# Kernel tuning notes

Hardware: AMD Instinct MI355X
Metric: run time of the kernel (lower is better)

## Reference

```python
import jax, jax.numpy as jnp
import numpy as np

B, N = 4096, 12
HID = 64
SLOPE = 0.2   # GATv2Conv default negative_slope
ALPHA = 0.1   # skip-connection scale


def _gabriel_adjacency(p):
    # p: [B, N, 2] node positions. Gabriel graph: edge (i,j) iff no other
    # point k lies inside the closed disk with diameter segment (p_i, p_j).
    n = p.shape[1]
    mid = (p[:, :, None, :] + p[:, None, :, :]) * 0.5                      # [B,N,N,2]
    r2 = jnp.sum((p[:, :, None, :] - p[:, None, :, :]) ** 2, -1) * 0.25    # [B,N,N]
    d2 = jnp.sum((p[:, None, None, :, :] - mid[:, :, :, None, :]) ** 2, -1)  # [B,i,j,k]
    eye = jnp.eye(n, dtype=bool)
    excl = eye[:, None, :] | eye[None, :, :]                               # k==i or k==j
    d2 = jnp.where(excl[None], jnp.inf, d2)
    gab = jnp.all(d2 > r2[..., None], axis=-1) & (~eye)[None]
    # undirected edges + self loops (GATv2Conv add_self_loops=True default)
    return gab | jnp.swapaxes(gab, 1, 2) | eye[None]                       # [B,N,N]


def _gatv2(x, adj, wl, wr, att, b):
    # PyG GATv2Conv, heads=1: e_ij = att . leaky_relu(W_l x_j + W_r x_i),
    # alpha = softmax_j(e_ij) over neighbors, out_i = sum_j alpha_ij W_l x_j + b.
    xl = x @ wl                                                            # source feats [B,N,H]
    xr = x @ wr                                                            # target feats [B,N,H]
    s = jax.nn.leaky_relu(xl[:, None, :, :] + xr[:, :, None, :], SLOPE)    # [B,i,j,H]
    e = jnp.einsum('bijh,h->bij', s, att)
    e = jnp.where(adj, e, -1e9)
    a = jax.nn.softmax(e, axis=-1)                                         # over sources j
    return jnp.einsum('bij,bjh->bih', a, xl) + b


def _forward(batch, enc_w1, enc_b1, enc_w2, enc_b2, enc_w3, enc_b3,
             g1_wl, g1_wr, g1_att, g1_b, g2_wl, g2_wr, g2_att, g2_b,
             g3_wl, g3_wr, g3_att, g3_b, g4_wl, g4_wr, g4_att, g4_b,
             lab_w, lab_b, val_w, val_b, skip_w, skip_b):
    h = jax.nn.relu(batch @ enc_w1 + enc_b1)
    h = jax.nn.relu(h @ enc_w2 + enc_b2)
    latent = h @ enc_w3 + enc_b3                                           # [B,N,3]
    # graph construction is non-differentiable (scipy in the original)
    adj = _gabriel_adjacency(jax.lax.stop_gradient(latent[..., :2]))
    x0 = latent[..., 2:3]                                                  # [B,N,1]
    x1 = jax.nn.relu(_gatv2(x0, adj, g1_wl, g1_wr, g1_att, g1_b))
    x2 = jax.nn.relu(_gatv2(x1, adj, g2_wl, g2_wr, g2_att, g2_b))
    skip = latent @ skip_w + skip_b
    x3 = jax.nn.relu(_gatv2(x2, adj, g3_wl, g3_wr, g3_att, g3_b) + ALPHA * skip)
    logits = x3 @ lab_w + lab_b                                            # [B,N,4]
    # note: original feeds x2 (not x3) into gcn4 -- kept faithful
    x4 = jax.nn.relu(_gatv2(x2, adj, g4_wl, g4_wr, g4_att, g4_b) + ALPHA * skip)
    values = x4 @ val_w + val_b                                            # [B,N,1]
    return batch[:, :, :4], batch[:, :, 4:5], logits, values, latent


def setup_inputs():
    key = jax.random.key(0)
    ks = iter(jax.random.split(key, 40))
    def rnd(shape, s=0.1):
        return jax.random.normal(next(ks), shape, dtype=jnp.float32) * s
    inp = {"batch": jax.random.normal(next(ks), (B, N, 5), dtype=jnp.float32)}
    inp.update(enc_w1=rnd((5, HID)), enc_b1=jnp.zeros((HID,), jnp.float32),
               enc_w2=rnd((HID, HID)), enc_b2=jnp.zeros((HID,), jnp.float32),
               enc_w3=rnd((HID, 3)), enc_b3=jnp.zeros((3,), jnp.float32))
    for i, cin in zip((1, 2, 3, 4), (1, HID, HID, HID)):
        inp[f"g{i}_wl"] = rnd((cin, HID)); inp[f"g{i}_wr"] = rnd((cin, HID))
        inp[f"g{i}_att"] = rnd((HID,)); inp[f"g{i}_b"] = jnp.zeros((HID,), jnp.float32)
    inp.update(lab_w=rnd((HID, 4)), lab_b=jnp.zeros((4,), jnp.float32),
               val_w=rnd((HID, 1)), val_b=jnp.zeros((1,), jnp.float32),
               skip_w=rnd((3, HID)), skip_b=jnp.zeros((HID,), jnp.float32))
    return inp


def reference(batch, enc_w1, enc_b1, enc_w2, enc_b2, enc_w3, enc_b3,
              g1_wl, g1_wr, g1_att, g1_b, g2_wl, g2_wr, g2_att, g2_b,
              g3_wl, g3_wr, g3_att, g3_b, g4_wl, g4_wr, g4_att, g4_b,
              lab_w, lab_b, val_w, val_b, skip_w, skip_b):
    return _forward(batch, enc_w1, enc_b1, enc_w2, enc_b2, enc_w3, enc_b3,
                    g1_wl, g1_wr, g1_att, g1_b, g2_wl, g2_wr, g2_att, g2_b,
                    g3_wl, g3_wr, g3_att, g3_b, g4_wl, g4_wr, g4_att, g4_b,
                    lab_w, lab_b, val_w, val_b, skip_w, skip_b)
```

## Files before the change

kernel.cpp:

```cpp
#include <hip/hip_runtime.h>
#include <hip/hip_bf16.h>
#include <math.h>

#define N     12
#define HID   64
#define STP   68
#define SLOPE 0.2f
#define ALPHA 0.1f

typedef float v2f __attribute__((ext_vector_type(2)));
typedef float v4f __attribute__((ext_vector_type(4)));
typedef int   i4  __attribute__((ext_vector_type(4)));
typedef short v8s __attribute__((ext_vector_type(8)));

static __device__ __forceinline__ v8s as_v8s(i4 v) {
    union { i4 a; v8s b; } u; u.a = v; return u.b;
}

#define OUT0 0
#define OUT1 196608
#define OUT2 245760
#define OUT3 442368
#define OUT4 491520

__global__ void prep_kernel(const float* __restrict__ enc_w2,
                            const float* __restrict__ g2_wl, const float* __restrict__ g2_wr,
                            const float* __restrict__ g3_wl, const float* __restrict__ g3_wr,
                            const float* __restrict__ g4_wl, const float* __restrict__ g4_wr,
                            const float* __restrict__ lab_w,
                            float* __restrict__ ws) {
    int t = threadIdx.x;
    int bx = blockIdx.x;
    if (bx < 64) {
        int c = bx;
        ws[t*64 + c] = enc_w2[c*64 + t];
        return;
    }
    if (bx == 112) {
        #pragma unroll
        for (int c = 0; c < 4; c++) ws[16384 + c*64 + t] = lab_w[t*4 + c];
        return;
    }
    int idx = bx - 64;
    int mat = idx >> 3, rem = idx & 7;
    int kt = rem >> 2, nt = rem & 3;
    const float* src;
    switch (mat) {
        case 0: src = g2_wl; break;
        case 1: src = g2_wr; break;
        case 2: src = g3_wl; break;
        case 3: src = g3_wr; break;
        case 4: src = g4_wl; break;
        default: src = g4_wr; break;
    }
    int quad = t >> 4, col = t & 15;
    int n = nt*16 + col;
    unsigned* dst = (unsigned*)(ws + 4096) + mat*2048 + (kt*4+nt)*256 + t*4;
    #pragma unroll
    for (int jp = 0; jp < 4; jp++) {
        int k0 = kt*32 + quad*8 + 2*jp;
        __hip_bfloat16 h0 = __float2bfloat16(src[(k0+0)*64 + n]);
        __hip_bfloat16 h1 = __float2bfloat16(src[(k0+1)*64 + n]);
        unsigned u0 = *(unsigned short*)&h0, u1 = *(unsigned short*)&h1;
        dst[jp] = u0 | (u1 << 16);
    }
}

template<bool TW>
__global__ __launch_bounds__(64, 3) void gae_kernel(
    const float* __restrict__ batch,
    const float* __restrict__ enc_w1, const float* __restrict__ enc_b1,
    const float* __restrict__ enc_w2, const float* __restrict__ enc_b2,
    const float* __restrict__ enc_w3, const float* __restrict__ enc_b3,
    const float* __restrict__ g1_wl, const float* __restrict__ g1_wr,
    const float* __restrict__ g1_att, const float* __restrict__ g1_b,
    const float* __restrict__ g2_wl, const float* __restrict__ g2_wr,
    const float* __restrict__ g2_att, const float* __restrict__ g2_b,
    const float* __restrict__ g3_wl, const float* __restrict__ g3_wr,
    const float* __restrict__ g3_att, const float* __restrict__ g3_b,
    const float* __restrict__ g4_wl, const float* __restrict__ g4_wr,
    const float* __restrict__ g4_att, const float* __restrict__ g4_b,
    const float* __restrict__ lab_w, const float* __restrict__ lab_b,
    const float* __restrict__ val_w, const float* __restrict__ val_b,
    const float* __restrict__ skip_w, const float* __restrict__ skip_b,
    const float* __restrict__ wsT,
    float* __restrict__ out)
{
    const int b = blockIdx.x;
    const int t = threadIdx.x;

    __shared__ __align__(16) float lds[2560];
    float* bufL = lds;
    float* bufR = lds + N*STP;
    float* xB   = lds + 2*N*STP;
    float* pool = lds + 2*N*STP + N*HID;
    unsigned char* pairs8 = (unsigned char*)&lds[2544];

    const v2f z2 = {0.f, 0.f};
    const v4f z4 = {0.f, 0.f, 0.f, 0.f};
    const v4f s4 = {SLOPE, SLOPE, SLOPE, SLOPE};

    const int p0 = t,        i0 = p0 / N, j0 = p0 - i0*N;
    const int p1 = t + 64,   i1 = p1 / N, j1 = p1 - i1*N;
    const int p2 = (t < 16) ? (t + 128) : 143;
    const int i2 = p2 / N,   j2 = p2 - i2*N;

    if (t < N*5) {
        float v = batch[b*(N*5) + t];
        pool[t] = v;
        int i = t / 5, f = t - i*5;
        if (f < 4) out[OUT0 + (size_t)b*(N*4) + i*4 + f] = v;
        else       out[OUT1 + (size_t)b*N + i] = v;
    }

    {
        float acc[N];
        float bias = enc_b1[t];
        #pragma unroll
        for (int i=0;i<N;i++) acc[i] = bias;
        #pragma unroll
        for (int f=0; f<5; f++) {
            float w = enc_w1[f*HID + t];
            #pragma unroll
            for (int i=0;i<N;i++) acc[i] = fmaf(pool[i*5+f], w, acc[i]);
        }
        #pragma unroll
        for (int i=0;i<N;i++) bufL[i*STP + t] = fmaxf(acc[i], 0.f);
    }

    {
        v2f acc[N];
        #pragma unroll
        for (int i=0;i<N;i++) acc[i] = z2;
        const float* w2p = TW ? (wsT + t*HID) : nullptr;
        for (int c=0;c<HID;c+=4) {
            v2f w01, w23;
            if (TW) {
                v4f w4 = *reinterpret_cast<const v4f*>(&w2p[c]);
                w01 = w4.xy; w23 = w4.zw;
            } else {
                w01 = (v2f){enc_w2[(c+0)*HID+t], enc_w2[(c+1)*HID+t]};
                w23 = (v2f){enc_w2[(c+2)*HID+t], enc_w2[(c+3)*HID+t]};
            }
            #pragma unroll
            for (int i=0;i<N;i++) {
                v4f xv = *reinterpret_cast<const v4f*>(&bufL[i*STP + c]);
                acc[i] = __builtin_elementwise_fma(xv.xy, w01, acc[i]);
                acc[i] = __builtin_elementwise_fma(xv.zw, w23, acc[i]);
            }
        }
        float bias = enc_b2[t];
        #pragma unroll
        for (int i=0;i<N;i++) bufR[i*STP + t] = fmaxf(bias + acc[i].x + acc[i].y, 0.f);
    }

    if (t < N*3) {
        int i = t / 3, c = t - i*3;
        float acc = enc_b3[c];
        for (int k=0;k<HID;k+=4) {
            v4f xv = *reinterpret_cast<const v4f*>(&bufR[i*STP + k]);
            acc = fmaf(xv.x, enc_w3[(k+0)*3+c], acc);
            acc = fmaf(xv.y, enc_w3[(k+1)*3+c], acc);
            acc = fmaf(xv.z, enc_w3[(k+2)*3+c], acc);
            acc = fmaf(xv.w, enc_w3[(k+3)*3+c], acc);
        }
        pool[t] = acc;
        out[OUT4 + (size_t)b*(N*3) + t] = acc;
    }

    float skipv[N];
    {
        float w0 = skip_w[t], w1 = skip_w[HID+t], w2 = skip_w[2*HID+t];
        float bias = skip_b[t];
        #pragma unroll
        for (int i=0;i<N;i++) {
            float v = bias;
            v = fmaf(pool[i*3+0], w0, v);
            v = fmaf(pool[i*3+1], w1, v);
            v = fmaf(pool[i*3+2], w2, v);
            skipv[i] = v;
        }
    }

    auto gab = [&](int i, int j)->bool {
        if (i == j) return false;
        float pix = pool[i*3], piy = pool[i*3+1];
        float pjx = pool[j*3], pjy = pool[j*3+1];
        float mx = (pix + pjx) * 0.5f, my = (piy + pjy) * 0.5f;
        float dx = pix - pjx, dy = piy - pjy;
        float r2 = (dx*dx + dy*dy) * 0.25f;
        bool g = true;
        #pragma unroll
        for (int k=0;k<N;k++) {
            float ex = pool[k*3] - mx, ey = pool[k*3+1] - my;
            bool ok = (k == i) || (k == j) || (ex*ex + ey*ey > r2);
            g = g && ok;
        }
        return g;
    };
    unsigned long long gb0 = __ballot(gab(i0, j0));
    unsigned long long gb1 = __ballot(gab(i1, j1));
    unsigned long long gb2 = __ballot((t < 16) && gab(i2, j2));
    auto gbit = [&](int p)->int {
        unsigned long long m = (p < 64) ? gb0 : ((p < 128) ? gb1 : gb2);
        return (int)((m >> (p & 63)) & 1ull);
    };
    const int adjA = gbit(p0) | gbit(j0*N+i0) | (i0 == j0);
    const int adjB = gbit(p1) | gbit(j1*N+i1) | (i1 == j1);
    const int adjC = (t < 16) ? (gbit(p2) | gbit(j2*N+i2) | (i2 == j2)) : 0;

    auto mbcnt64 = [&](unsigned long long m)->int {
        return __builtin_amdgcn_mbcnt_hi((unsigned)(m >> 32),
               __builtin_amdgcn_mbcnt_lo((unsigned)m, 0));
    };
    const unsigned long long am0 = __ballot(adjA != 0);
    const unsigned long long am1 = __ballot(adjB != 0);
    const unsigned long long am2 = __ballot(adjC != 0);
    const int c0  = __popcll(am0);
    const int c01 = c0 + __popcll(am1);
    const int nv  = c01 + __popcll(am2);
    const int idx0 = mbcnt64(am0);
    const int idx1 = c0  + mbcnt64(am1);
    const int idx2 = c01 + mbcnt64(am2);
    if (adjA)               pairs8[idx0] = (unsigned char)p0;
    if (adjB && idx1 < 64)  pairs8[idx1] = (unsigned char)p1;
    if (adjC && idx2 < 64)  pairs8[idx2] = (unsigned char)p2;
    const bool ovB = adjB && (idx1 >= 64);
    const bool ovC = adjC && (idx2 >= 64);
    const int nvc = nv < 64 ? nv : 64;

    auto scoreAt = [&](int i, int j, const float* __restrict__ att)->float {
        const float* Lj = &bufL[j*STP];
        const float* Ri = &bufR[i*STP];
        v4f a0 = z4, a1 = z4;
        for (int h=0; h<HID; h+=8) {
            v4f t0 = *reinterpret_cast<const v4f*>(&att[h]);
            v4f t1 = *reinterpret_cast<const v4f*>(&att[h+4]);
            v4f xl0 = *reinterpret_cast<const v4f*>(Lj + h);
            v4f xl1 = *reinterpret_cast<const v4f*>(Lj + h + 4);
            v4f xr0 = *reinterpret_cast<const v4f*>(Ri + h);
            v4f xr1 = *reinterpret_cast<const v4f*>(Ri + h + 4);
            v4f s0 = xl0 + xr0;
            v4f s1 = xl1 + xr1;
            v4f l0 = __builtin_elementwise_fma(s4, __builtin_elementwise_min(s0, z4),
                                               __builtin_elementwise_max(s0, z4));
            v4f l1 = __builtin_elementwise_fma(s4, __builtin_elementwise_min(s1, z4),
                                               __builtin_elementwise_max(s1, z4));
            a0 = __builtin_elementwise_fma(t0, l0, a0);
            a1 = __builtin_elementwise_fma(t1, l1, a1);
        }
        v4f a = a0 + a1;
        return (a.x + a.y) + (a.z + a.w);
    };

    auto gat_core = [&](const float* __restrict__ att, const float* __restrict__ gb,
                        float* __restrict__ xout, int strideOut, int useSkip) {
        pool[t] = -1e9f; pool[t+64] = -1e9f;
        if (t < 16) pool[t+128] = -1e9f;
        if (t < nvc) {
            int p = pairs8[t];
            int i = (p * 171) >> 11;
            int j = p - i*N;
            pool[p] = scoreAt(i, j, att);
        }
        if (nv > 64) {
            if (ovB) pool[p1] = scoreAt(i1, j1, att);
            if (ovC) pool[p2] = scoreAt(i2, j2, att);
        }
        float xj[N];
        #pragma unroll
        for (int j=0;j<N;j++) xj[j] = bufL[j*STP + t];
        float bias = gb[t];
        if (t < N) {
            float m = -2e9f;
            #pragma unroll
            for (int j=0;j<N;j++) m = fmaxf(m, pool[t*N+j]);
            float tmp[N]; float sum = 0.f;
            #pragma unroll
            for (int j=0;j<N;j++) { float v = __expf(pool[t*N+j] - m); tmp[j] = v; sum += v; }
            float inv = 1.0f / sum;
            #pragma unroll
            for (int j=0;j<N;j++) pool[t*N+j] = tmp[j] * inv;
        }
        {
            v4f X0 = {xj[0], xj[1], xj[2],  xj[3]};
            v4f X1 = {xj[4], xj[5], xj[6],  xj[7]};
            v4f X2 = {xj[8], xj[9], xj[10], xj[11]};
            #pragma unroll
            for (int i=0;i<N;i++) {
                const v4f* ep = reinterpret_cast<const v4f*>(&pool[i*N]);
                v4f acc = __builtin_elementwise_fma(ep[0], X0,
                          __builtin_elementwise_fma(ep[1], X1, ep[2]*X2));
                float r = bias + ((acc.x + acc.y) + (acc.z + acc.w));
                if (useSkip) r = fmaf(ALPHA, skipv[i], r);
                xout[i*strideOut + t] = fmaxf(r, 0.f);
            }
        }
    };

    auto stage_mfma = [&](const float* __restrict__ xin, int strideIn, int matL) {
        const int m = t & 15, quad = t >> 4;
        const int mc = (m < N) ? m : 0;
        i4 aF[2];
        #pragma unroll
        for (int kt=0; kt<2; kt++) {
            const float* xp = &xin[mc*strideIn + kt*32 + quad*8];
            v4f lo = *reinterpret_cast<const v4f*>(xp);
            v4f hi = *reinterpret_cast<const v4f*>(xp + 4);
            unsigned u0 = __float_as_uint(lo.x) + 0x8000u, u1 = __float_as_uint(lo.y) + 0x8000u;
            unsigned u2 = __float_as_uint(lo.z) + 0x8000u, u3 = __float_as_uint(lo.w) + 0x8000u;
            unsigned u4 = __float_as_uint(hi.x) + 0x8000u, u5 = __float_as_uint(hi.y) + 0x8000u;
            unsigned u6 = __float_as_uint(hi.z) + 0x8000u, u7 = __float_as_uint(hi.w) + 0x8000u;
            i4 a;
            a.x = (int)__builtin_amdgcn_perm(u1, u0, 0x07060302u);
            a.y = (int)__builtin_amdgcn_perm(u3, u2, 0x07060302u);
            a.z = (int)__builtin_amdgcn_perm(u5, u4, 0x07060302u);
            a.w = (int)__builtin_amdgcn_perm(u7, u6, 0x07060302u);
            aF[kt] = a;
        }
        const i4* bbase = reinterpret_cast<const i4*>(wsT + 4096);
        #pragma unroll
        for (int mm=0; mm<2; mm++) {
            const i4* bp = bbase + (matL + mm)*512;
            v4f acc[4] = {z4, z4, z4, z4};
            #pragma unroll
            for (int nt=0; nt<4; nt++) {
                i4 b0 = bp[(0*4+nt)*64 + t];
                i4 b1 = bp[(1*4+nt)*64 + t];
                acc[nt] = __builtin_amdgcn_mfma_f32_16x16x32_bf16(as_v8s(aF[0]), as_v8s(b0), acc[nt], 0, 0, 0);
                acc[nt] = __builtin_amdgcn_mfma_f32_16x16x32_bf16(as_v8s(aF[1]), as_v8s(b1), acc[nt], 0, 0, 0);
            }
            float* dst = (mm == 0) ? bufL : bufR;
            if (quad < 3) {
                #pragma unroll
                for (int nt=0; nt<4; nt++) {
                    #pragma unroll
                    for (int r=0; r<4; r++)
                        dst[(quad*4+r)*STP + nt*16 + m] = acc[nt][r];
                }
            }
        }
    };

    auto stage = [&](const float* __restrict__ xin, int strideIn,
                     const float* __restrict__ wl, const float* __restrict__ wr) {
        v2f al[N], ar[N];
        #pragma unroll
        for (int i=0;i<N;i++) { al[i] = z2; ar[i] = z2; }
        for (int c=0;c<HID;c+=4) {
            v2f wl01 = (v2f){wl[(c+0)*HID+t], wl[(c+1)*HID+t]};
            v2f wl23 = (v2f){wl[(c+2)*HID+t], wl[(c+3)*HID+t]};
            v2f wr01 = (v2f){wr[(c+0)*HID+t], wr[(c+1)*HID+t]};
            v2f wr23 = (v2f){wr[(c+2)*HID+t], wr[(c+3)*HID+t]};
            #pragma unroll
            for (int i=0;i<N;i++) {
                v4f xv = *reinterpret_cast<const v4f*>(&xin[i*strideIn + c]);
                al[i] = __builtin_elementwise_fma(xv.xy, wl01, al[i]);
                al[i] = __builtin_elementwise_fma(xv.zw, wl23, al[i]);
                ar[i] = __builtin_elementwise_fma(xv.xy, wr01, ar[i]);
                ar[i] = __builtin_elementwise_fma(xv.zw, wr23, ar[i]);
            }
        }
        #pragma unroll
        for (int i=0;i<N;i++) {
            bufL[i*STP + t] = al[i].x + al[i].y;
            bufR[i*STP + t] = ar[i].x + ar[i].y;
        }
    };

    {
        float wlv = g1_wl[t], wrv = g1_wr[t];
        #pragma unroll
        for (int i=0;i<N;i++) {
            float v = pool[i*3+2];
            bufL[i*STP + t] = v * wlv;
            bufR[i*STP + t] = v * wrv;
        }
    }
    gat_core(g1_att, g1_b, bufR, STP, 0);

    if (TW) stage_mfma(bufR, STP, 0); else stage(bufR, STP, g2_wl, g2_wr);
    gat_core(g2_att, g2_b, xB, HID, 0);

    if (TW) stage_mfma(xB, HID, 2); else stage(xB, HID, g3_wl, g3_wr);
    gat_core(g3_att, g3_b, bufR, STP, 1);

    if (t < N*4) {
        int i = t >> 2, c = t & 3;
        float acc = lab_b[c];
        if (TW) {
            const float* lwT = wsT + 16384 + c*HID;
            for (int h=0;h<HID;h+=4) {
                v4f xv = *reinterpret_cast<const v4f*>(&bufR[i*STP + h]);
                v4f w4 = *reinterpret_cast<const v4f*>(&lwT[h]);
                acc = fmaf(xv.x, w4.x, acc);
                acc = fmaf(xv.y, w4.y, acc);
                acc = fmaf(xv.z, w4.z, acc);
                acc = fmaf(xv.w, w4.w, acc);
            }
        } else {
            for (int h=0;h<HID;h+=4) {
                v4f xv = *reinterpret_cast<const v4f*>(&bufR[i*STP + h]);
                acc = fmaf(xv.x, lab_w[(h+0)*4+c], acc);
                acc = fmaf(xv.y, lab_w[(h+1)*4+c], acc);
                acc = fmaf(xv.z, lab_w[(h+2)*4+c], acc);
                acc = fmaf(xv.w, lab_w[(h+3)*4+c], acc);
            }
        }
        out[OUT2 + (size_t)b*(N*4) + t] = acc;
    }

    if (TW) stage_mfma(xB, HID, 4); else stage(xB, HID, g4_wl, g4_wr);
    gat_core(g4_att, g4_b, bufR, STP, 1);

    if (t < N) {
        float acc = val_b[0];
        for (int h=0;h<HID;h+=4) {
            v4f xv = *reinterpret_cast<const v4f*>(&bufR[t*STP + h]);
            v4f w4 = *reinterpret_cast<const v4f*>(&val_w[h]);
            acc = fmaf(xv.x, w4.x, acc);
            acc = fmaf(xv.y, w4.y, acc);
            acc = fmaf(xv.z, w4.z, acc);
            acc = fmaf(xv.w, w4.w, acc);
        }
        out[OUT3 + (size_t)b*N + t] = acc;
    }
}

extern "C" void kernel_launch(void* const* d_in, const int* in_sizes, int n_in,
                              void* d_out, int out_size, void* d_ws, size_t ws_size,
                              hipStream_t stream) {
    (void)in_sizes; (void)n_in; (void)out_size;
    const bool useT = (ws_size >= (16384 + 256)*sizeof(float));
    if (useT) {
        prep_kernel<<<dim3(113), dim3(64), 0, stream>>>(
            (const float*)d_in[3],
            (const float*)d_in[11], (const float*)d_in[12],
            (const float*)d_in[15], (const float*)d_in[16],
            (const float*)d_in[19], (const float*)d_in[20],
            (const float*)d_in[23],
            (float*)d_ws);
        gae_kernel<true><<<dim3(4096), dim3(64), 0, stream>>>(
            (const float*)d_in[0],
            (const float*)d_in[1],  (const float*)d_in[2],
            (const float*)d_in[3],  (const float*)d_in[4],
            (const float*)d_in[5],  (const float*)d_in[6],
            (const float*)d_in[7],  (const float*)d_in[8],  (const float*)d_in[9],  (const float*)d_in[10],
            (const float*)d_in[11], (const float*)d_in[12], (const float*)d_in[13], (const float*)d_in[14],
            (const float*)d_in[15], (const float*)d_in[16], (const float*)d_in[17], (const float*)d_in[18],
            (const float*)d_in[19], (const float*)d_in[20], (const float*)d_in[21], (const float*)d_in[22],
            (const float*)d_in[23], (const float*)d_in[24],
            (const float*)d_in[25], (const float*)d_in[26],
            (const float*)d_in[27], (const float*)d_in[28],
            (const float*)d_ws,
            (float*)d_out);
    } else {
        gae_kernel<false><<<dim3(4096), dim3(64), 0, stream>>>(
            (const float*)d_in[0],
            (const float*)d_in[1],  (const float*)d_in[2],
            (const float*)d_in[3],  (const float*)d_in[4],
            (const float*)d_in[5],  (const float*)d_in[6],
            (const float*)d_in[7],  (const float*)d_in[8],  (const float*)d_in[9],  (const float*)d_in[10],
            (const float*)d_in[11], (const float*)d_in[12], (const float*)d_in[13], (const float*)d_in[14],
            (const float*)d_in[15], (const float*)d_in[16], (const float*)d_in[17], (const float*)d_in[18],
            (const float*)d_in[19], (const float*)d_in[20], (const float*)d_in[21], (const float*)d_in[22],
            (const float*)d_in[23], (const float*)d_in[24],
            (const float*)d_in[25], (const float*)d_in[26],
            (const float*)d_in[27], (const float*)d_in[28],
            nullptr,
            (float*)d_out);
    }
}
```

Before: 153.3 us.

## Process two graphs per wavefront to amortize weight loads and latency

Each 64-thread block now handles two batch samples, with duplicated LDS buffers and interleaved computation for both graphs at every stage (encoder, Gabriel adjacency, GAT attention, MFMA projections, heads). This amortizes weight fetches and MFMA B-operand loads across two samples and exposes more instruction-level parallelism per wave. The grid is halved to 2048 blocks and launch bounds relaxed to 2 waves per SIMD. It doubles LDS and register use, which lowers occupancy and leaves fewer blocks to spread across the GPU's compute units. The leaky-relu is also rewritten as max(s, s*slope).

New measurement: 159.4 us. 4.0% more time.

```diff
diff --git a/kernel.cpp b/kernel.cpp
--- a/kernel.cpp
+++ b/kernel.cpp
@@ -67,7 +67,7 @@
 }
 
 template<bool TW>
-__global__ __launch_bounds__(64, 3) void gae_kernel(
+__global__ __launch_bounds__(64, 2) void gae_kernel(
     const float* __restrict__ batch,
     const float* __restrict__ enc_w1, const float* __restrict__ enc_b1,
     const float* __restrict__ enc_w2, const float* __restrict__ enc_b2,
@@ -86,17 +86,17 @@
     const float* __restrict__ wsT,
     float* __restrict__ out)
 {
-    const int b = blockIdx.x;
+    const int bb = blockIdx.x * 2;
     const int t = threadIdx.x;
 
-    __shared__ __align__(16) float lds[2560];
-    float* bufL = lds;
-    float* bufR = lds + N*STP;
-    float* xB   = lds + 2*N*STP;
-    float* pool = lds + 2*N*STP + N*HID;
-    unsigned char* pairs8 = (unsigned char*)&lds[2544];
-
-    const v2f z2 = {0.f, 0.f};
+    __shared__ __align__(16) float lds[5120];
+    float* bufL0 = lds;            float* bufL1 = lds + 2560;
+    float* bufR0 = lds + 816;      float* bufR1 = lds + 2560 + 816;
+    float* xB0   = lds + 1632;     float* xB1   = lds + 2560 + 1632;
+    float* pool0 = lds + 2400;     float* pool1 = lds + 2560 + 2400;
+    unsigned char* pr0 = (unsigned char*)(lds + 2544);
+    unsigned char* pr1 = (unsigned char*)(lds + 2560 + 2544);
+
     const v4f z4 = {0.f, 0.f, 0.f, 0.f};
     const v4f s4 = {SLOPE, SLOPE, SLOPE, SLOPE};
 
@@ -106,32 +106,47 @@
     const int i2 = p2 / N,   j2 = p2 - i2*N;
 
     if (t < N*5) {
-        float v = batch[b*(N*5) + t];
-        pool[t] = v;
         int i = t / 5, f = t - i*5;
-        if (f < 4) out[OUT0 + (size_t)b*(N*4) + i*4 + f] = v;
-        else       out[OUT1 + (size_t)b*N + i] = v;
+        float v0 = batch[(size_t)(bb+0)*(N*5) + t];
+        float v1 = batch[(size_t)(bb+1)*(N*5) + t];
+        pool0[t] = v0;
+        pool1[t] = v1;
+        if (f < 4) {
+            out[OUT0 + (size_t)(bb+0)*(N*4) + i*4 + f] = v0;
+            out[OUT0 + (size_t)(bb+1)*(N*4) + i*4 + f] = v1;
+        } else {
+            out[OUT1 + (size_t)(bb+0)*N + i] = v0;
+            out[OUT1 + (size_t)(bb+1)*N + i] = v1;
+        }
     }
 
     {
-        float acc[N];
+        float w[5];
+        #pragma unroll
+        for (int f=0; f<5; f++) w[f] = enc_w1[f*HID + t];
         float bias = enc_b1[t];
-        #pragma unroll
-        for (int i=0;i<N;i++) acc[i] = bias;
+        float a0[N], a1[N];
+        #pragma unroll
+        for (int i=0;i<N;i++) { a0[i] = bias; a1[i] = bias; }
         #pragma unroll
         for (int f=0; f<5; f++) {
-            float w = enc_w1[f*HID + t];
-            #pragma unroll
-            for (int i=0;i<N;i++) acc[i] = fmaf(pool[i*5+f], w, acc[i]);
-        }
-        #pragma unroll
-        for (int i=0;i<N;i++) bufL[i*STP + t] = fmaxf(acc[i], 0.f);
+            #pragma unroll
+            for (int i=0;i<N;i++) {
+                a0[i] = fmaf(pool0[i*5+f], w[f], a0[i]);
+                a1[i] = fmaf(pool1[i*5+f], w[f], a1[i]);
+            }
+        }
+        #pragma unroll
+        for (int i=0;i<N;i++) {
+            bufL0[i*STP + t] = fmaxf(a0[i], 0.f);
+            bufL1[i*STP + t] = fmaxf(a1[i], 0.f);
+        }
     }
 
     {
-        v2f acc[N];
-        #pragma unroll
-        for (int i=0;i<N;i++) acc[i] = z2;
+        v2f a0[N], a1[N];
+        #pragma unroll
+        for (int i=0;i<N;i++) { a0[i] = (v2f){0.f,0.f}; a1[i] = (v2f){0.f,0.f}; }
         const float* w2p = TW ? (wsT + t*HID) : nullptr;
         for (int c=0;c<HID;c+=4) {
             v2f w01, w23;
@@ -144,94 +159,167 @@
             }
             #pragma unroll
             for (int i=0;i<N;i++) {
-                v4f xv = *reinterpret_cast<const v4f*>(&bufL[i*STP + c]);
-                acc[i] = __builtin_elementwise_fma(xv.xy, w01, acc[i]);
-                acc[i] = __builtin_elementwise_fma(xv.zw, w23, acc[i]);
+                v4f x0 = *reinterpret_cast<const v4f*>(&bufL0[i*STP + c]);
+                v4f x1 = *reinterpret_cast<const v4f*>(&bufL1[i*STP + c]);
+                a0[i] = __builtin_elementwise_fma(x0.xy, w01, a0[i]);
+                a0[i] = __builtin_elementwise_fma(x0.zw, w23, a0[i]);
+                a1[i] = __builtin_elementwise_fma(x1.xy, w01, a1[i]);
+                a1[i] = __builtin_elementwise_fma(x1.zw, w23, a1[i]);
             }
         }
         float bias = enc_b2[t];
         #pragma unroll
-        for (int i=0;i<N;i++) bufR[i*STP + t] = fmaxf(bias + acc[i].x + acc[i].y, 0.f);
+        for (int i=0;i<N;i++) {
+            bufR0[i*STP + t] = fmaxf(bias + a0[i].x + a0[i].y, 0.f);
+            bufR1[i*STP + t] = fmaxf(bias + a1[i].x + a1[i].y, 0.f);
+        }
     }
 
     if (t < N*3) {
         int i = t / 3, c = t - i*3;
-        float acc = enc_b3[c];
+        float b3 = enc_b3[c];
+        float a0 = b3, a1 = b3;
         for (int k=0;k<HID;k+=4) {
-            v4f xv = *reinterpret_cast<const v4f*>(&bufR[i*STP + k]);
-            acc = fmaf(xv.x, enc_w3[(k+0)*3+c], acc);
-            acc = fmaf(xv.y, enc_w3[(k+1)*3+c], acc);
-            acc = fmaf(xv.z, enc_w3[(k+2)*3+c], acc);
-            acc = fmaf(xv.w, enc_w3[(k+3)*3+c], acc);
-        }
-        pool[t] = acc;
-        out[OUT4 + (size_t)b*(N*3) + t] = acc;
-    }
-
-    float skipv[N];
+            float w0 = enc_w3[(k+0)*3+c], w1 = enc_w3[(k+1)*3+c];
+            float w2 = enc_w3[(k+2)*3+c], w3 = enc_w3[(k+3)*3+c];
+            v4f x0 = *reinterpret_cast<const v4f*>(&bufR0[i*STP + k]);
+            v4f x1 = *reinterpret_cast<const v4f*>(&bufR1[i*STP + k]);
+            a0 = fmaf(x0.x, w0, a0); a0 = fmaf(x0.y, w1, a0);
+            a0 = fmaf(x0.z, w2, a0); a0 = fmaf(x0.w, w3, a0);
+            a1 = fmaf(x1.x, w0, a1); a1 = fmaf(x1.y, w1, a1);
+            a1 = fmaf(x1.z, w2, a1); a1 = fmaf(x1.w, w3, a1);
+        }
+        pool0[t] = a0;
+        pool1[t] = a1;
+        out[OUT4 + (size_t)(bb+0)*(N*3) + t] = a0;
+        out[OUT4 + (size_t)(bb+1)*(N*3) + t] = a1;
+    }
+
+    float skv0[N], skv1[N];
     {
         float w0 = skip_w[t], w1 = skip_w[HID+t], w2 = skip_w[2*HID+t];
         float bias = skip_b[t];
         #pragma unroll
         for (int i=0;i<N;i++) {
-            float v = bias;
-            v = fmaf(pool[i*3+0], w0, v);
-            v = fmaf(pool[i*3+1], w1, v);
-            v = fmaf(pool[i*3+2], w2, v);
-            skipv[i] = v;
-        }
-    }
-
-    auto gab = [&](int i, int j)->bool {
+            float v0 = bias, v1 = bias;
+            v0 = fmaf(pool0[i*3+0], w0, v0); v1 = fmaf(pool1[i*3+0], w0, v1);
+            v0 = fmaf(pool0[i*3+1], w1, v0); v1 = fmaf(pool1[i*3+1], w1, v1);
+            v0 = fmaf(pool0[i*3+2], w2, v0); v1 = fmaf(pool1[i*3+2], w2, v1);
+            skv0[i] = v0; skv1[i] = v1;
+        }
+    }
+
+    auto gab = [&](const float* __restrict__ po, int i, int j)->bool {
         if (i == j) return false;
-        float pix = pool[i*3], piy = pool[i*3+1];
-        float pjx = pool[j*3], pjy = pool[j*3+1];
+        float pix = po[i*3], piy = po[i*3+1];
+        float pjx = po[j*3], pjy = po[j*3+1];
         float mx = (pix + pjx) * 0.5f, my = (piy + pjy) * 0.5f;
         float dx = pix - pjx, dy = piy - pjy;
         float r2 = (dx*dx + dy*dy) * 0.25f;
         bool g = true;
         #pragma unroll
         for (int k=0;k<N;k++) {
-            float ex = pool[k*3] - mx, ey = pool[k*3+1] - my;
+            float ex = po[k*3] - mx, ey = po[k*3+1] - my;
             bool ok = (k == i) || (k == j) || (ex*ex + ey*ey > r2);
             g = g && ok;
         }
         return g;
     };
-    unsigned long long gb0 = __ballot(gab(i0, j0));
-    unsigned long long gb1 = __ballot(gab(i1, j1));
-    unsigned long long gb2 = __ballot((t < 16) && gab(i2, j2));
-    auto gbit = [&](int p)->int {
-        unsigned long long m = (p < 64) ? gb0 : ((p < 128) ? gb1 : gb2);
+    const unsigned long long gA0 = __ballot(gab(pool0, i0, j0));
+    const unsigned long long gA1 = __ballot(gab(pool1, i0, j0));
+    const unsigned long long gB0 = __ballot(gab(pool0, i1, j1));
+    const unsigned long long gB1 = __ballot(gab(pool1, i1, j1));
+    const unsigned long long gC0 = __ballot((t < 16) && gab(pool0, i2, j2));
+    const unsigned long long gC1 = __ballot((t < 16) && gab(pool1, i2, j2));
+    auto gbit0 = [&](int p)->int {
+        unsigned long long m = (p < 64) ? gA0 : ((p < 128) ? gB0 : gC0);
         return (int)((m >> (p & 63)) & 1ull);
     };
-    const int adjA = gbit(p0) | gbit(j0*N+i0) | (i0 == j0);
-    const int adjB = gbit(p1) | gbit(j1*N+i1) | (i1 == j1);
-    const int adjC = (t < 16) ? (gbit(p2) | gbit(j2*N+i2) | (i2 == j2)) : 0;
-
+    auto gbit1 = [&](int p)->int {
+        unsigned long long m = (p < 64) ? gA1 : ((p < 128) ? gB1 : gC1);
+        return (int)((m >> (p & 63)) & 1ull);
+    };
     auto mbcnt64 = [&](unsigned long long m)->int {
         return __builtin_amdgcn_mbcnt_hi((unsigned)(m >> 32),
                __builtin_amdgcn_mbcnt_lo((unsigned)m, 0));
     };
-    const unsigned long long am0 = __ballot(adjA != 0);
-    const unsigned long long am1 = __ballot(adjB != 0);
-    const unsigned long long am2 = __ballot(adjC != 0);
-    const int c0  = __popcll(am0);
-    const int c01 = c0 + __popcll(am1);
-    const int nv  = c01 + __popcll(am2);
-    const int idx0 = mbcnt64(am0);
-    const int idx1 = c0  + mbcnt64(am1);
-    const int idx2 = c01 + mbcnt64(am2);
-    if (adjA)               pairs8[idx0] = (unsigned char)p0;
-    if (adjB && idx1 < 64)  pairs8[idx1] = (unsigned char)p1;
-    if (adjC && idx2 < 64)  pairs8[idx2] = (unsigned char)p2;
-    const bool ovB = adjB && (idx1 >= 64);
-    const bool ovC = adjC && (idx2 >= 64);
-    const int nvc = nv < 64 ? nv : 64;
-
-    auto scoreAt = [&](int i, int j, const float* __restrict__ att)->float {
-        const float* Lj = &bufL[j*STP];
-        const float* Ri = &bufR[i*STP];
+
+    int nv0, nvc0; bool ovB0, ovC0;
+    {
+        int adjA = gbit0(p0) | gbit0(j0*N+i0) | (i0 == j0);
+        int adjB = gbit0(p1) | gbit0(j1*N+i1) | (i1 == j1);
+        int adjC = (t < 16) ? (gbit0(p2) | gbit0(j2*N+i2) | (i2 == j2)) : 0;
+        unsigned long long am0 = __ballot(adjA != 0);
+        unsigned long long am1 = __ballot(adjB != 0);
+        unsigned long long am2 = __ballot(adjC != 0);
+        int c0  = __popcll(am0);
+        int c01 = c0 + __popcll(am1);
+        nv0 = c01 + __popcll(am2);
+        int ix0 = mbcnt64(am0);
+        int ix1 = c0  + mbcnt64(am1);
+        int ix2 = c01 + mbcnt64(am2);
+        if (adjA)               pr0[ix0] = (unsigned char)p0;
+        if (adjB && ix1 < 64)   pr0[ix1] = (unsigned char)p1;
+        if (adjC && ix2 < 64)   pr0[ix2] = (unsigned char)p2;
+        ovB0 = adjB && (ix1 >= 64);
+        ovC0 = adjC && (ix2 >= 64);
+        nvc0 = nv0 < 64 ? nv0 : 64;
+    }
+    int nv1, nvc1; bool ovB1, ovC1;
+    {
+        int adjA = gbit1(p0) | gbit1(j0*N+i0) | (i0 == j0);
+        int adjB = gbit1(p1) | gbit1(j1*N+i1) | (i1 == j1);
+        int adjC = (t < 16) ? (gbit1(p2) | gbit1(j2*N+i2) | (i2 == j2)) : 0;
+        unsigned long long am0 = __ballot(adjA != 0);
+        unsigned long long am1 = __ballot(adjB != 0);
+        unsigned long long am2 = __ballot(adjC != 0);
+        int c0  = __popcll(am0);
+        int c01 = c0 + __popcll(am1);
+        nv1 = c01 + __popcll(am2);
+        int ix0 = mbcnt64(am0);
+        int ix1 = c0  + mbcnt64(am1);
+        int ix2 = c01 + mbcnt64(am2);
+        if (adjA)               pr1[ix0] = (unsigned char)p0;
+        if (adjB && ix1 < 64)   pr1[ix1] = (unsigned char)p1;
+        if (adjC && ix2 < 64)   pr1[ix2] = (unsigned char)p2;
+        ovB1 = adjB && (ix1 >= 64);
+        ovC1 = adjC && (ix2 >= 64);
+        nvc1 = nv1 < 64 ? nv1 : 64;
+    }
+
+    auto score2 = [&](int ia0, int ja0, int ia1, int ja1,
+                      const float* __restrict__ att, float& r0, float& r1) {
+        const float* L0 = &bufL0[ja0*STP];
+        const float* R0 = &bufR0[ia0*STP];
+        const float* L1 = &bufL1[ja1*STP];
+        const float* R1 = &bufR1[ia1*STP];
+        v4f a0 = z4, a1 = z4, b0 = z4, b1 = z4;
+        for (int h=0; h<HID; h+=8) {
+            v4f t0 = *reinterpret_cast<const v4f*>(&att[h]);
+            v4f t1 = *reinterpret_cast<const v4f*>(&att[h+4]);
+            v4f xl00 = *reinterpret_cast<const v4f*>(L0 + h);
+            v4f xl01 = *reinterpret_cast<const v4f*>(L0 + h + 4);
+            v4f xr00 = *reinterpret_cast<const v4f*>(R0 + h);
+            v4f xr01 = *reinterpret_cast<const v4f*>(R0 + h + 4);
+            v4f xl10 = *reinterpret_cast<const v4f*>(L1 + h);
+            v4f xl11 = *reinterpret_cast<const v4f*>(L1 + h + 4);
+            v4f xr10 = *reinterpret_cast<const v4f*>(R1 + h);
+            v4f xr11 = *reinterpret_cast<const v4f*>(R1 + h + 4);
+            v4f s00 = xl00 + xr00, s01 = xl01 + xr01;
+            v4f s10 = xl10 + xr10, s11 = xl11 + xr11;
+            a0 = __builtin_elementwise_fma(t0, __builtin_elementwise_max(s00, s00 * s4), a0);
+            a1 = __builtin_elementwise_fma(t1, __builtin_elementwise_max(s01, s01 * s4), a1);
+            b0 = __builtin_elementwise_fma(t0, __builtin_elementwise_max(s10, s10 * s4), b0);
+            b1 = __builtin_elementwise_fma(t1, __builtin_elementwise_max(s11, s11 * s4), b1);
+        }
+        v4f A = a0 + a1, B = b0 + b1;
+        r0 = (A.x + A.y) + (A.z + A.w);
+        r1 = (B.x + B.y) + (B.z + B.w);
+    };
+    auto scoreS = [&](const float* __restrict__ bL, const float* __restrict__ bR,
+                      int i, int j, const float* __restrict__ att)->float {
+        const float* Lj = &bL[j*STP];
+        const float* Ri = &bR[i*STP];
         v4f a0 = z4, a1 = z4;
         for (int h=0; h<HID; h+=8) {
             v4f t0 = *reinterpret_cast<const v4f*>(&att[h]);
@@ -240,68 +328,91 @@
             v4f xl1 = *reinterpret_cast<const v4f*>(Lj + h + 4);
             v4f xr0 = *reinterpret_cast<const v4f*>(Ri + h);
             v4f xr1 = *reinterpret_cast<const v4f*>(Ri + h + 4);
-            v4f s0 = xl0 + xr0;
-            v4f s1 = xl1 + xr1;
-            v4f l0 = __builtin_elementwise_fma(s4, __builtin_elementwise_min(s0, z4),
-                                               __builtin_elementwise_max(s0, z4));
-            v4f l1 = __builtin_elementwise_fma(s4, __builtin_elementwise_min(s1, z4),
-                                               __builtin_elementwise_max(s1, z4));
-            a0 = __builtin_elementwise_fma(t0, l0, a0);
-            a1 = __builtin_elementwise_fma(t1, l1, a1);
+            v4f s0 = xl0 + xr0, s1 = xl1 + xr1;
+            a0 = __builtin_elementwise_fma(t0, __builtin_elementwise_max(s0, s0 * s4), a0);
+            a1 = __builtin_elementwise_fma(t1, __builtin_elementwise_max(s1, s1 * s4), a1);
         }
         v4f a = a0 + a1;
         return (a.x + a.y) + (a.z + a.w);
     };
 
-    auto gat_core = [&](const float* __restrict__ att, const float* __restrict__ gb,
-                        float* __restrict__ xout, int strideOut, int useSkip) {
-        pool[t] = -1e9f; pool[t+64] = -1e9f;
-        if (t < 16) pool[t+128] = -1e9f;
-        if (t < nvc) {
-            int p = pairs8[t];
-            int i = (p * 171) >> 11;
-            int j = p - i*N;
-            pool[p] = scoreAt(i, j, att);
-        }
-        if (nv > 64) {
-            if (ovB) pool[p1] = scoreAt(i1, j1, att);
-            if (ovC) pool[p2] = scoreAt(i2, j2, att);
-        }
-        float xj[N];
-        #pragma unroll
-        for (int j=0;j<N;j++) xj[j] = bufL[j*STP + t];
-        float bias = gb[t];
+    auto gat_core2 = [&](const float* __restrict__ att, const float* __restrict__ gbias,
+                         float* __restrict__ xo0, float* __restrict__ xo1,
+                         int strideOut, int useSkip) {
+        pool0[t] = -1e9f; pool0[t+64] = -1e9f;
+        pool1[t] = -1e9f; pool1[t+64] = -1e9f;
+        if (t < 16) { pool0[t+128] = -1e9f; pool1[t+128] = -1e9f; }
+        {
+            int q0 = pr0[(t < nvc0) ? t : 0];
+            int q1 = pr1[(t < nvc1) ? t : 0];
+            int ia0 = (q0*171) >> 11, ja0 = q0 - ia0*N;
+            int ia1 = (q1*171) >> 11, ja1 = q1 - ia1*N;
+            float s0, s1;
+            score2(ia0, ja0, ia1, ja1, att, s0, s1);
+            if (t < nvc0) pool0[q0] = s0;
+            if (t < nvc1) pool1[q1] = s1;
+            if (nv0 > 64) {
+                if (ovB0) pool0[p1] = scoreS(bufL0, bufR0, i1, j1, att);
+                if (ovC0) pool0[p2] = scoreS(bufL0, bufR0, i2, j2, att);
+            }
+            if (nv1 > 64) {
+                if (ovB1) pool1[p1] = scoreS(bufL1, bufR1, i1, j1, att);
+                if (ovC1) pool1[p2] = scoreS(bufL1, bufR1, i2, j2, att);
+            }
+        }
+        float xj0[N], xj1[N];
+        #pragma unroll
+        for (int j=0;j<N;j++) { xj0[j] = bufL0[j*STP + t]; xj1[j] = bufL1[j*STP + t]; }
+        float bias = gbias[t];
         if (t < N) {
-            float m = -2e9f;
-            #pragma unroll
-            for (int j=0;j<N;j++) m = fmaxf(m, pool[t*N+j]);
-            float tmp[N]; float sum = 0.f;
-            #pragma unroll
-            for (int j=0;j<N;j++) { float v = __expf(pool[t*N+j] - m); tmp[j] = v; sum += v; }
-            float inv = 1.0f / sum;
-            #pragma unroll
-            for (int j=0;j<N;j++) pool[t*N+j] = tmp[j] * inv;
+            float m0 = -2e9f, m1 = -2e9f;
+            #pragma unroll
+            for (int j=0;j<N;j++) {
+                m0 = fmaxf(m0, pool0[t*N+j]);
+                m1 = fmaxf(m1, pool1[t*N+j]);
+            }
+            float t0[N], t1[N]; float su0 = 0.f, su1 = 0.f;
+            #pragma unroll
+            for (int j=0;j<N;j++) {
+                float e0 = __expf(pool0[t*N+j] - m0);
+                float e1 = __expf(pool1[t*N+j] - m1);
+                t0[j] = e0; su0 += e0;
+                t1[j] = e1; su1 += e1;
+            }
+            float iv0 = 1.0f / su0, iv1 = 1.0f / su1;
+            #pragma unroll
+            for (int j=0;j<N;j++) {
+                pool0[t*N+j] = t0[j] * iv0;
+                pool1[t*N+j] = t1[j] * iv1;
+            }
         }
         {
-            v4f X0 = {xj[0], xj[1], xj[2],  xj[3]};
-            v4f X1 = {xj[4], xj[5], xj[6],  xj[7]};
-            v4f X2 = {xj[8], xj[9], xj[10], xj[11]};
+            v4f X00 = {xj0[0], xj0[1], xj0[2],  xj0[3]};
+            v4f X01 = {xj0[4], xj0[5], xj0[6],  xj0[7]};
+            v4f X02 = {xj0[8], xj0[9], xj0[10], xj0[11]};
+            v4f X10 = {xj1[0], xj1[1], xj1[2],  xj1[3]};
+            v4f X11 = {xj1[4], xj1[5], xj1[6],  xj1[7]};
+            v4f X12 = {xj1[8], xj1[9], xj1[10], xj1[11]};
             #pragma unroll
             for (int i=0;i<N;i++) {
-                const v4f* ep = reinterpret_cast<const v4f*>(&pool[i*N]);
-                v4f acc = __builtin_elementwise_fma(ep[0], X0,
-                          __builtin_elementwise_fma(ep[1], X1, ep[2]*X2));
-                float r = bias + ((acc.x + acc.y) + (acc.z + acc.w));
-                if (useSkip) r = fmaf(ALPHA, skipv[i], r);
-                xout[i*strideOut + t] = fmaxf(r, 0.f);
-            }
-        }
-    };
-
-    auto stage_mfma = [&](const float* __restrict__ xin, int strideIn, int matL) {
+                const v4f* e0 = reinterpret_cast<const v4f*>(&pool0[i*N]);
+                const v4f* e1 = reinterpret_cast<const v4f*>(&pool1[i*N]);
+                v4f a0 = __builtin_elementwise_fma(e0[0], X00,
+                         __builtin_elementwise_fma(e0[1], X01, e0[2]*X02));
+                v4f a1 = __builtin_elementwise_fma(e1[0], X10,
+                         __builtin_elementwise_fma(e1[1], X11, e1[2]*X12));
+                float r0 = bias + ((a0.x + a0.y) + (a0.z + a0.w));
+                float r1 = bias + ((a1.x + a1.y) + (a1.z + a1.w));
+                if (useSkip) { r0 = fmaf(ALPHA, skv0[i], r0); r1 = fmaf(ALPHA, skv1[i], r1); }
+                xo0[i*strideOut + t] = fmaxf(r0, 0.f);
+                xo1[i*strideOut + t] = fmaxf(r1, 0.f);
+            }
+        }
+    };
+
+    auto packA = [&](const float* __restrict__ xin, int strideIn, i4* aF) {
         const int m = t & 15, quad = t >> 4;
         const int mc = (m < N) ? m : 0;
-        i4 aF[2];
         #pragma unroll
         for (int kt=0; kt<2; kt++) {
             const float* xp = &xin[mc*strideIn + kt*32 + quad*8];
@@ -318,35 +429,50 @@
             a.w = (int)__builtin_amdgcn_perm(u7, u6, 0x07060302u);
             aF[kt] = a;
         }
+    };
+
+    auto stage_mfma2 = [&](const float* __restrict__ x0, const float* __restrict__ x1,
+                           int strideIn, int matL) {
+        const int m = t & 15, quad = t >> 4;
+        i4 aF0[2], aF1[2];
+        packA(x0, strideIn, aF0);
+        packA(x1, strideIn, aF1);
         const i4* bbase = reinterpret_cast<const i4*>(wsT + 4096);
         #pragma unroll
         for (int mm=0; mm<2; mm++) {
             const i4* bp = bbase + (matL + mm)*512;
-            v4f acc[4] = {z4, z4, z4, z4};
+            v4f ac0[4] = {z4, z4, z4, z4};
+            v4f ac1[4] = {z4, z4, z4, z4};
             #pragma unroll
             for (int nt=0; nt<4; nt++) {
-                i4 b0 = bp[(0*4+nt)*64 + t];
-                i4 b1 = bp[(1*4+nt)*64 + t];
-                acc[nt] = __builtin_amdgcn_mfma_f32_16x16x32_bf16(as_v8s(aF[0]), as_v8s(b0), acc[nt], 0, 0, 0);
-                acc[nt] = __builtin_amdgcn_mfma_f32_16x16x32_bf16(as_v8s(aF[1]), as_v8s(b1), acc[nt], 0, 0, 0);
-            }
-            float* dst = (mm == 0) ? bufL : bufR;
+                i4 b0 = bp[nt*64 + t];
+                i4 b1 = bp[(4+nt)*64 + t];
+                ac0[nt] = __builtin_amdgcn_mfma_f32_16x16x32_bf16(as_v8s(aF0[0]), as_v8s(b0), ac0[nt], 0, 0, 0);
+                ac0[nt] = __builtin_amdgcn_mfma_f32_16x16x32_bf16(as_v8s(aF0[1]), as_v8s(b1), ac0[nt], 0, 0, 0);
+                ac1[nt] = __builtin_amdgcn_mfma_f32_16x16x32_bf16(as_v8s(aF1[0]), as_v8s(b0), ac1[nt], 0, 0, 0);
+                ac1[nt] = __builtin_amdgcn_mfma_f32_16x16x32_bf16(as_v8s(aF1[1]), as_v8s(b1), ac1[nt], 0, 0, 0);
+            }
+            float* d0 = mm ? bufR0 : bufL0;
+            float* d1 = mm ? bufR1 : bufL1;
             if (quad < 3) {
                 #pragma unroll
                 for (int nt=0; nt<4; nt++) {
                     #pragma unroll
-                    for (int r=0; r<4; r++)
-                        dst[(quad*4+r)*STP + nt*16 + m] = acc[nt][r];
+                    for (int r=0; r<4; r++) {
+                        d0[(quad*4+r)*STP + nt*16 + m] = ac0[nt][r];
+                        d1[(quad*4+r)*STP + nt*16 + m] = ac1[nt][r];
+                    }
                 }
             }
         }
     };
 
-    auto stage = [&](const float* __restrict__ xin, int strideIn,
-                     const float* __restrict__ wl, const float* __restrict__ wr) {
+    auto stage_f32 = [&](const float* __restrict__ xin, int strideIn,
+                         const float* __restrict__ wl, const float* __restrict__ wr,
+                         float* __restrict__ dL, float* __restrict__ dR) {
         v2f al[N], ar[N];
         #pragma unroll
-        for (int i=0;i<N;i++) { al[i] = z2; ar[i] = z2; }
+        for (int i=0;i<N;i++) { al[i] = (v2f){0.f,0.f}; ar[i] = (v2f){0.f,0.f}; }
         for (int c=0;c<HID;c+=4) {
             v2f wl01 = (v2f){wl[(c+0)*HID+t], wl[(c+1)*HID+t]};
             v2f wl23 = (v2f){wl[(c+2)*HID+t], wl[(c+3)*HID+t]};
@@ -363,8 +489,8 @@
         }
         #pragma unroll
         for (int i=0;i<N;i++) {
-            bufL[i*STP + t] = al[i].x + al[i].y;
-            bufR[i*STP + t] = ar[i].x + ar[i].y;
+            dL[i*STP + t] = al[i].x + al[i].y;
+            dR[i*STP + t] = ar[i].x + ar[i].y;
         }
     };
 
@@ -372,58 +498,73 @@
         float wlv = g1_wl[t], wrv = g1_wr[t];
         #pragma unroll
         for (int i=0;i<N;i++) {
-            float v = pool[i*3+2];
-            bufL[i*STP + t] = v * wlv;
-            bufR[i*STP + t] = v * wrv;
-        }
-    }
-    gat_core(g1_att, g1_b, bufR, STP, 0);
-
-    if (TW) stage_mfma(bufR, STP, 0); else stage(bufR, STP, g2_wl, g2_wr);
-    gat_core(g2_att, g2_b, xB, HID, 0);
-
-    if (TW) stage_mfma(xB, HID, 2); else stage(xB, HID, g3_wl, g3_wr);
-    gat_core(g3_att, g3_b, bufR, STP, 1);
+            float v0 = pool0[i*3+2], v1 = pool1[i*3+2];
+            bufL0[i*STP + t] = v0 * wlv;  bufR0[i*STP + t] = v0 * wrv;
+            bufL1[i*STP + t] = v1 * wlv;  bufR1[i*STP + t] = v1 * wrv;
+        }
+    }
+    gat_core2(g1_att, g1_b, bufR0, bufR1, STP, 0);
+
+    if (TW) stage_mfma2(bufR0, bufR1, STP, 0);
+    else { stage_f32(bufR0, STP, g2_wl, g2_wr, bufL0, bufR0);
+           stage_f32(bufR1, STP, g2_wl, g2_wr, bufL1, bufR1); }
+    gat_core2(g2_att, g2_b, xB0, xB1, HID, 0);
+
+    if (TW) stage_mfma2(xB0, xB1, HID, 2);
+    else { stage_f32(xB0, HID, g3_wl, g3_wr, bufL0, bufR0);
+           stage_f32(xB1, HID, g3_wl, g3_wr, bufL1, bufR1); }
+    gat_core2(g3_att, g3_b, bufR0, bufR1, STP, 1);
 
     if (t < N*4) {
         int i = t >> 2, c = t & 3;
-        float acc = lab_b[c];
+        float lb = lab_b[c];
+        float a0 = lb, a1 = lb;
         if (TW) {
             const float* lwT = wsT + 16384 + c*HID;
             for (int h=0;h<HID;h+=4) {
-                v4f xv = *reinterpret_cast<const v4f*>(&bufR[i*STP + h]);
                 v4f w4 = *reinterpret_cast<const v4f*>(&lwT[h]);
-                acc = fmaf(xv.x, w4.x, acc);
-                acc = fmaf(xv.y, w4.y, acc);
-                acc = fmaf(xv.z, w4.z, acc);
-                acc = fmaf(xv.w, w4.w, acc);
+                v4f x0 = *reinterpret_cast<const v4f*>(&bufR0[i*STP + h]);
+                v4f x1 = *reinterpret_cast<const v4f*>(&bufR1[i*STP + h]);
+                a0 = fmaf(x0.x, w4.x, a0); a0 = fmaf(x0.y, w4.y, a0);
+                a0 = fmaf(x0.z, w4.z, a0); a0 = fmaf(x0.w, w4.w, a0);
+                a1 = fmaf(x1.x, w4.x, a1); a1 = fmaf(x1.y, w4.y, a1);
+                a1 = fmaf(x1.z, w4.z, a1); a1 = fmaf(x1.w, w4.w, a1);
             }
         } else {
             for (int h=0;h<HID;h+=4) {
-                v4f xv = *reinterpret_cast<const v4f*>(&bufR[i*STP + h]);
-                acc = fmaf(xv.x, lab_w[(h+0)*4+c], acc);
-                acc = fmaf(xv.y, lab_w[(h+1)*4+c], acc);
-                acc = fmaf(xv.z, lab_w[(h+2)*4+c], acc);
-                acc = fmaf(xv.w, lab_w[(h+3)*4+c], acc);
-            }
-        }
-        out[OUT2 + (size_t)b*(N*4) + t] = acc;
-    }
-
-    if (TW) stage_mfma(xB, HID, 4); else stage(xB, HID, g4_wl, g4_wr);
-    gat_core(g4_att, g4_b, bufR, STP, 1);
+                float w0 = lab_w[(h+0)*4+c], w1 = lab_w[(h+1)*4+c];
+                float w2 = lab_w[(h+2)*4+c], w3 = lab_w[(h+3)*4+c];
+                v4f x0 = *reinterpret_cast<const v4f*>(&bufR0[i*STP + h]);
+                v4f x1 = *reinterpret_cast<const v4f*>(&bufR1[i*STP + h]);
+                a0 = fmaf(x0.x, w0, a0); a0 = fmaf(x0.y, w1, a0);
+                a0 = fmaf(x0.z, w2, a0); a0 = fmaf(x0.w, w3, a0);
+                a1 = fmaf(x1.x, w0, a1); a1 = fmaf(x1.y, w1, a1);
+                a1 = fmaf(x1.z, w2, a1); a1 = fmaf(x1.w, w3, a1);
+            }
+        }
+        out[OUT2 + (size_t)(bb+0)*(N*4) + t] = a0;
+        out[OUT2 + (size_t)(bb+1)*(N*4) + t] = a1;
+    }
+
+    if (TW) stage_mfma2(xB0, xB1, HID, 4);
+    else { stage_f32(xB0, HID, g4_wl, g4_wr, bufL0, bufR0);
+           stage_f32(xB1, HID, g4_wl, g4_wr, bufL1, bufR1); }
+    gat_core2(g4_att, g4_b, bufR0, bufR1, STP, 1);
 
     if (t < N) {
-        float acc = val_b[0];
+        float vb = val_b[0];
+        float a0 = vb, a1 = vb;
         for (int h=0;h<HID;h+=4) {
-            v4f xv = *reinterpret_cast<const v4f*>(&bufR[t*STP + h]);
             v4f w4 = *reinterpret_cast<const v4f*>(&val_w[h]);
-            acc = fmaf(xv.x, w4.x, acc);
-            acc = fmaf(xv.y, w4.y, acc);
-            acc = fmaf(xv.z, w4.z, acc);
-            acc = fmaf(xv.w, w4.w, acc);
-        }
-        out[OUT3 + (size_t)b*N + t] = acc;
+            v4f x0 = *reinterpret_cast<const v4f*>(&bufR0[t*STP + h]);
+            v4f x1 = *reinterpret_cast<const v4f*>(&bufR1[t*STP + h]);
+            a0 = fmaf(x0.x, w4.x, a0); a0 = fmaf(x0.y, w4.y, a0);
+            a0 = fmaf(x0.z, w4.z, a0); a0 = fmaf(x0.w, w4.w, a0);
+            a1 = fmaf(x1.x, w4.x, a1); a1 = fmaf(x1.y, w4.y, a1);
+            a1 = fmaf(x1.z, w4.z, a1); a1 = fmaf(x1.w, w4.w, a1);
+        }
+        out[OUT3 + (size_t)(bb+0)*N + t] = a0;
+        out[OUT3 + (size_t)(bb+1)*N + t] = a1;
     }
 }
 
@@ -440,7 +581,7 @@
             (const float*)d_in[19], (const float*)d_in[20],
             (const float*)d_in[23],
             (float*)d_ws);
-        gae_kernel<true><<<dim3(4096), dim3(64), 0, stream>>>(
+        gae_kernel<true><<<dim3(2048), dim3(64), 0, stream>>>(
             (const float*)d_in[0],
             (const float*)d_in[1],  (const float*)d_in[2],
             (const float*)d_in[3],  (const float*)d_in[4],
@@ -455,7 +596,7 @@
             (const float*)d_ws,
             (float*)d_out);
     } else {
-        gae_kernel<false><<<dim3(4096), dim3(64), 0, stream>>>(
+        gae_kernel<false><<<dim3(2048), dim3(64), 0, stream>>>(
             (const float*)d_in[0],
             (const float*)d_in[1],  (const float*)d_in[2],
             (const float*)d_in[3],  (const float*)d_in[4],
```
